# Kernel tuning notes

Measured on AMD Instinct MI355X. Metric: run time of the kernel, lower is better.

Reference implementation:

```python
import jax, jax.numpy as jnp
import numpy as np

B, P, DE, DD, DA = 256, 196, 2048, 512, 512

def setup_inputs() -> dict:
    key = jax.random.key(0)
    ks = jax.random.split(key, 8)
    s_enc = 1.0 / np.sqrt(DE)
    s_dec = 1.0 / np.sqrt(DD)
    s_att = 1.0 / np.sqrt(DA)
    return {
        "encoder_out": jax.random.normal(ks[0], (B, P, DE), dtype=jnp.float32),
        "decoder_hidden": jax.random.normal(ks[1], (B, DD), dtype=jnp.float32),
        "W_enc": jax.random.uniform(ks[2], (DE, DA), jnp.float32, -s_enc, s_enc),
        "b_enc": jax.random.uniform(ks[3], (DA,), jnp.float32, -s_enc, s_enc),
        "W_dec": jax.random.uniform(ks[4], (DD, DA), jnp.float32, -s_dec, s_dec),
        "b_dec": jax.random.uniform(ks[5], (DA,), jnp.float32, -s_dec, s_dec),
        "W_full": jax.random.uniform(ks[6], (DA, 1), jnp.float32, -s_att, s_att),
        "b_full": jax.random.uniform(ks[7], (1,), jnp.float32, -s_att, s_att),
    }

def reference(encoder_out, decoder_hidden, W_enc, b_enc, W_dec, b_dec, W_full, b_full):
    # att1: [B,P,DA]; att2: [B,DA]
    att1 = jnp.einsum('bpe,ea->bpa', encoder_out, W_enc) + b_enc
    att2 = decoder_hidden @ W_dec + b_dec
    # broadcast add + relu + project to scalar score per position
    att = jnp.einsum('bpa,a->bp', jax.nn.relu(att1 + att2[:, None, :]), W_full[:, 0]) + b_full[0]
    alpha = jax.nn.softmax(att, axis=1)  # [B,P]
    context_vector = jnp.einsum('bpe,bp->be', encoder_out, alpha)  # [B,DE]
    return (context_vector, alpha)
```

## Files before the change

kernel.cpp:

```cpp
#include <hip/hip_runtime.h>
#include <hip/hip_bf16.h>
#include <cstddef>

#define B_   256
#define P_   196
#define DE_  2048
#define DD_  512
#define DA_  512
#define M_   (B_*P_)

#define BM   64
#define KT   32

typedef __attribute__((ext_vector_type(4))) float f32x4;
typedef __attribute__((ext_vector_type(8))) short s16x8;

__global__ void pack_wenc(const float* __restrict__ W, __hip_bfloat16* __restrict__ out) {
    __shared__ float lds[KT][128 + 1];
    const int kt = blockIdx.x;
    const int n0 = blockIdx.y * 128;
    const int t  = threadIdx.x;
#pragma unroll
    for (int i = 0; i < 16; ++i) {
        int e  = t + i * 256;
        int kl = e >> 7;
        int nl = e & 127;
        lds[kl][nl] = W[(size_t)(kt * KT + kl) * DA_ + n0 + nl];
    }
    __syncthreads();
#pragma unroll
    for (int i = 0; i < 16; ++i) {
        int e  = t + i * 256;
        int nl = e >> 5;
        int kk = e & 31;
        out[((size_t)kt * DA_ + n0 + nl) * KT + kk] = __float2bfloat16(lds[kk][nl]);
    }
}

__global__ __launch_bounds__(512) void att2_kernel(
        const float* __restrict__ dh, const float* __restrict__ W_dec,
        const float* __restrict__ b_dec, const float* __restrict__ b_enc,
        float* __restrict__ att2p) {
    __shared__ float s_dh[DD_];
    const int b = blockIdx.x;
    const int a = threadIdx.x;
    s_dh[a] = dh[(size_t)b * DD_ + a];
    __syncthreads();
    float acc = 0.f;
#pragma unroll 8
    for (int k = 0; k < DD_; ++k)
        acc += s_dh[k] * W_dec[(size_t)k * DA_ + a];
    att2p[(size_t)b * DA_ + a] = acc + b_dec[a] + b_enc[a];
}

__global__ __launch_bounds__(512, 1) void gemm_att(
        const float* __restrict__ enc, const __hip_bfloat16* __restrict__ Bp,
        const float* __restrict__ att2p, const float* __restrict__ Wfull,
        const float* __restrict__ bfull, float* __restrict__ att) {
    __shared__ __hip_bfloat16 a_lds[BM * KT];
    __shared__ __hip_bfloat16 b_lds[DA_ * KT];
    __shared__ float red[BM][8];

    const int tid  = threadIdx.x;
    const int wave = tid >> 6;
    const int lane = tid & 63;
    const int g    = lane >> 4;
    const int c    = lane & 15;
    const int block_row = blockIdx.x * BM;
    const int nbase = wave * 64;

    f32x4 acc[4][4] = {};

    for (int kt = 0; kt < DE_ / KT; ++kt) {
        __syncthreads();
        {
            const int r  = tid >> 3;
            const int kk = (tid & 7) * 4;
            const float* src = enc + (size_t)(block_row + r) * DE_ + kt * KT + kk;
            f32x4 v = *reinterpret_cast<const f32x4*>(src);
            __hip_bfloat16* d = a_lds + r * KT + kk;
            d[0] = __float2bfloat16(v.x);
            d[1] = __float2bfloat16(v.y);
            d[2] = __float2bfloat16(v.z);
            d[3] = __float2bfloat16(v.w);
        }
        {
            const s16x8* src = reinterpret_cast<const s16x8*>(Bp + (size_t)kt * DA_ * KT);
            s16x8* dst = reinterpret_cast<s16x8*>(b_lds);
#pragma unroll
            for (int i = 0; i < 4; ++i)
                dst[tid + i * 512] = src[tid + i * 512];
        }
        __syncthreads();
        s16x8 afrag[4], bfrag[4];
#pragma unroll
        for (int mt = 0; mt < 4; ++mt)
            afrag[mt] = *reinterpret_cast<const s16x8*>(a_lds + (mt * 16 + c) * KT + g * 8);
#pragma unroll
        for (int nt = 0; nt < 4; ++nt)
            bfrag[nt] = *reinterpret_cast<const s16x8*>(b_lds + (nbase + nt * 16 + c) * KT + g * 8);
#pragma unroll
        for (int mt = 0; mt < 4; ++mt)
#pragma unroll
            for (int nt = 0; nt < 4; ++nt)
                acc[mt][nt] = __builtin_amdgcn_mfma_f32_16x16x32_bf16(
                                  afrag[mt], bfrag[nt], acc[mt][nt], 0, 0, 0);
    }

#pragma unroll
    for (int mt = 0; mt < 4; ++mt) {
#pragma unroll
        for (int q = 0; q < 4; ++q) {
            const int row_local = mt * 16 + g * 4 + q;
            const int R = block_row + row_local;
            const int b = R / P_;
            float s = 0.f;
#pragma unroll
            for (int nt = 0; nt < 4; ++nt) {
                const int n = nbase + nt * 16 + c;
                float v = acc[mt][nt][q] + att2p[(size_t)b * DA_ + n];
                v = fmaxf(v, 0.f);
                s += v * Wfull[n];
            }
#pragma unroll
            for (int off = 1; off < 16; off <<= 1)
                s += __shfl_xor(s, off, 64);
            if (c == 0) red[row_local][wave] = s;
        }
    }
    __syncthreads();
    if (tid < BM) {
        float t = 0.f;
#pragma unroll
        for (int w = 0; w < 8; ++w) t += red[tid][w];
        att[block_row + tid] = t + bfull[0];
    }
}

__global__ __launch_bounds__(256) void softmax_kernel(
        const float* __restrict__ att, float* __restrict__ alpha) {
    const int b = blockIdx.x;
    const int t = threadIdx.x;
    __shared__ float sred[4];
    float v = (t < P_) ? att[(size_t)b * P_ + t] : -1e30f;
    float m = v;
#pragma unroll
    for (int off = 1; off < 64; off <<= 1) m = fmaxf(m, __shfl_xor(m, off, 64));
    if ((t & 63) == 0) sred[t >> 6] = m;
    __syncthreads();
    const float mall = fmaxf(fmaxf(sred[0], sred[1]), fmaxf(sred[2], sred[3]));
    __syncthreads();
    float e = (t < P_) ? expf(v - mall) : 0.f;
    float s = e;
#pragma unroll
    for (int off = 1; off < 64; off <<= 1) s += __shfl_xor(s, off, 64);
    if ((t & 63) == 0) sred[t >> 6] = s;
    __syncthreads();
    const float stot = sred[0] + sred[1] + sred[2] + sred[3];
    if (t < P_) alpha[(size_t)b * P_ + t] = e / stot;
}

__global__ __launch_bounds__(256) void context_kernel(
        const float* __restrict__ enc, const float* __restrict__ alpha,
        float* __restrict__ ctx) {
    const int b = blockIdx.x;
    const int e = blockIdx.y * 1024 + threadIdx.x * 4;
    __shared__ float s_alpha[P_];
    if (threadIdx.x < P_) s_alpha[threadIdx.x] = alpha[(size_t)b * P_ + threadIdx.x];
    __syncthreads();
    f32x4 acc = {0.f, 0.f, 0.f, 0.f};
    const float* base = enc + (size_t)b * P_ * DE_ + e;
#pragma unroll 4
    for (int p = 0; p < P_; ++p) {
        f32x4 v = *reinterpret_cast<const f32x4*>(base + (size_t)p * DE_);
        acc += s_alpha[p] * v;
    }
    *reinterpret_cast<f32x4*>(ctx + (size_t)b * DE_ + e) = acc;
}

extern "C" void kernel_launch(void* const* d_in, const int* in_sizes, int n_in,
                              void* d_out, int out_size, void* d_ws, size_t ws_size,
                              hipStream_t stream) {
    const float* enc    = (const float*)d_in[0];
    const float* dh     = (const float*)d_in[1];
    const float* W_enc  = (const float*)d_in[2];
    const float* b_enc  = (const float*)d_in[3];
    const float* W_dec  = (const float*)d_in[4];
    const float* b_dec  = (const float*)d_in[5];
    const float* W_full = (const float*)d_in[6];
    const float* b_full = (const float*)d_in[7];

    float* out       = (float*)d_out;
    float* ctx_out   = out;
    float* alpha_out = out + (size_t)B_ * DE_;

    char* ws = (char*)d_ws;
    __hip_bfloat16* Bp = (__hip_bfloat16*)ws;
    float* att2p = (float*)(ws + 2u * 1024 * 1024);
    float* att   = (float*)(ws + 2u * 1024 * 1024 + 512u * 1024);

    pack_wenc   <<<dim3(64, 4),   256, 0, stream>>>(W_enc, Bp);
    att2_kernel <<<B_,            512, 0, stream>>>(dh, W_dec, b_dec, b_enc, att2p);
    gemm_att    <<<M_ / BM,       512, 0, stream>>>(enc, Bp, att2p, W_full, b_full, att);
    softmax_kernel<<<B_,          256, 0, stream>>>(att, alpha_out);
    context_kernel<<<dim3(B_, 2), 256, 0, stream>>>(enc, alpha_out, ctx_out);
}
```

Before: 321.2 us.

## Enlarge GEMM row tile, swizzle LDS layout, and load B via global_load_lds

The M tile grows from 64 to 112 rows, so each block does 7x4 MFMA tiles and the shared W_enc tile is reused across more rows with fewer blocks. The packed W_enc and the A tile in LDS use an XOR swizzle on the 8-element slots to cut bank conflicts. B tiles are copied straight from global memory into LDS with global_load_lds, skipping the register round trip. The epilogue preloads W_full and the att2 rows for the at most two batches a tile spans, and launch bounds now allow two blocks per CU. The risks are higher register pressure from 28 accumulator tiles and unused threads during the A load.

Measured after the change: 312.1 us. 1.03x faster.

```diff
diff --git a/kernel.cpp b/kernel.cpp
--- a/kernel.cpp
+++ b/kernel.cpp
@@ -9,11 +9,20 @@
 #define DA_  512
 #define M_   (B_*P_)
 
-#define BM   64
+#define BM   112
 #define KT   32
 
 typedef __attribute__((ext_vector_type(4))) float f32x4;
 typedef __attribute__((ext_vector_type(8))) short s16x8;
+
+static __device__ __forceinline__ short f2bf(float x) {
+    __hip_bfloat16 h = __float2bfloat16(x);
+    return *reinterpret_cast<short*>(&h);
+}
+
+#define GLOAD_LDS16(g, l) __builtin_amdgcn_global_load_lds( \
+    (const __attribute__((address_space(1))) void*)(g),     \
+    (__attribute__((address_space(3))) void*)(l), 16, 0, 0)
 
 __global__ void pack_wenc(const float* __restrict__ W, __hip_bfloat16* __restrict__ out) {
     __shared__ float lds[KT][128 + 1];
@@ -28,12 +37,19 @@
         lds[kl][nl] = W[(size_t)(kt * KT + kl) * DA_ + n0 + nl];
     }
     __syncthreads();
-#pragma unroll
-    for (int i = 0; i < 16; ++i) {
-        int e  = t + i * 256;
-        int nl = e >> 5;
-        int kk = e & 31;
-        out[((size_t)kt * DA_ + n0 + nl) * KT + kk] = __float2bfloat16(lds[kk][nl]);
+    short* o16 = reinterpret_cast<short*>(out);
+#pragma unroll
+    for (int i = 0; i < 2; ++i) {
+        int task = t + i * 256;
+        int nl   = task >> 2;
+        int s    = task & 3;
+        int n    = n0 + nl;
+        int sp   = s ^ ((n >> 1) & 3);
+        s16x8 w;
+#pragma unroll
+        for (int j = 0; j < 8; ++j)
+            w[j] = f2bf(lds[s * 8 + j][nl]);
+        *reinterpret_cast<s16x8*>(o16 + (size_t)kt * (DA_ * KT) + n * KT + sp * 8) = w;
     }
 }
 
@@ -53,7 +69,7 @@
     att2p[(size_t)b * DA_ + a] = acc + b_dec[a] + b_enc[a];
 }
 
-__global__ __launch_bounds__(512, 1) void gemm_att(
+__global__ __launch_bounds__(512, 2) void gemm_att(
         const float* __restrict__ enc, const __hip_bfloat16* __restrict__ Bp,
         const float* __restrict__ att2p, const float* __restrict__ Wfull,
         const float* __restrict__ bfull, float* __restrict__ att) {
@@ -69,58 +85,74 @@
     const int block_row = blockIdx.x * BM;
     const int nbase = wave * 64;
 
-    f32x4 acc[4][4] = {};
+    const int slot8 = (g ^ ((c >> 1) & 3)) * 8;
+
+    const int ar = tid >> 2;
+    const int aq = tid & 3;
+    const bool a_active = (tid < BM * 4);
+    __hip_bfloat16* a_dst = a_lds + ar * KT + (aq ^ ((ar >> 1) & 3)) * 8;
+    const float* a_src = enc + (size_t)(block_row + ar) * DE_ + aq * 8;
+
+    f32x4 acc[7][4] = {};
 
     for (int kt = 0; kt < DE_ / KT; ++kt) {
         __syncthreads();
         {
-            const int r  = tid >> 3;
-            const int kk = (tid & 7) * 4;
-            const float* src = enc + (size_t)(block_row + r) * DE_ + kt * KT + kk;
-            f32x4 v = *reinterpret_cast<const f32x4*>(src);
-            __hip_bfloat16* d = a_lds + r * KT + kk;
-            d[0] = __float2bfloat16(v.x);
-            d[1] = __float2bfloat16(v.y);
-            d[2] = __float2bfloat16(v.z);
-            d[3] = __float2bfloat16(v.w);
+            const char* bsrc = (const char*)Bp + (size_t)kt * (DA_ * KT * 2) + (size_t)tid * 16;
+            char*       bdst = (char*)b_lds + wave * 1024;
+#pragma unroll
+            for (int i = 0; i < 4; ++i)
+                GLOAD_LDS16(bsrc + i * 8192, bdst + i * 8192);
         }
-        {
-            const s16x8* src = reinterpret_cast<const s16x8*>(Bp + (size_t)kt * DA_ * KT);
-            s16x8* dst = reinterpret_cast<s16x8*>(b_lds);
-#pragma unroll
-            for (int i = 0; i < 4; ++i)
-                dst[tid + i * 512] = src[tid + i * 512];
+        if (a_active) {
+            f32x4 v0 = *reinterpret_cast<const f32x4*>(a_src + kt * KT);
+            f32x4 v1 = *reinterpret_cast<const f32x4*>(a_src + kt * KT + 4);
+            s16x8 w;
+            w[0] = f2bf(v0.x); w[1] = f2bf(v0.y); w[2] = f2bf(v0.z); w[3] = f2bf(v0.w);
+            w[4] = f2bf(v1.x); w[5] = f2bf(v1.y); w[6] = f2bf(v1.z); w[7] = f2bf(v1.w);
+            *reinterpret_cast<s16x8*>(a_dst) = w;
         }
         __syncthreads();
-        s16x8 afrag[4], bfrag[4];
-#pragma unroll
-        for (int mt = 0; mt < 4; ++mt)
-            afrag[mt] = *reinterpret_cast<const s16x8*>(a_lds + (mt * 16 + c) * KT + g * 8);
+        s16x8 afrag[7], bfrag[4];
+#pragma unroll
+        for (int mt = 0; mt < 7; ++mt)
+            afrag[mt] = *reinterpret_cast<const s16x8*>(a_lds + (mt * 16 + c) * KT + slot8);
 #pragma unroll
         for (int nt = 0; nt < 4; ++nt)
-            bfrag[nt] = *reinterpret_cast<const s16x8*>(b_lds + (nbase + nt * 16 + c) * KT + g * 8);
-#pragma unroll
-        for (int mt = 0; mt < 4; ++mt)
+            bfrag[nt] = *reinterpret_cast<const s16x8*>(b_lds + (nbase + nt * 16 + c) * KT + slot8);
+#pragma unroll
+        for (int mt = 0; mt < 7; ++mt)
 #pragma unroll
             for (int nt = 0; nt < 4; ++nt)
                 acc[mt][nt] = __builtin_amdgcn_mfma_f32_16x16x32_bf16(
                                   afrag[mt], bfrag[nt], acc[mt][nt], 0, 0, 0);
     }
 
-#pragma unroll
-    for (int mt = 0; mt < 4; ++mt) {
+    const int b0    = block_row / P_;
+    const int b1    = min(b0 + 1, B_ - 1);
+    const int split = (b0 + 1) * P_;
+    float wf[4], a20[4], a21[4];
+#pragma unroll
+    for (int nt = 0; nt < 4; ++nt) {
+        const int n = nbase + nt * 16 + c;
+        wf[nt]  = Wfull[n];
+        a20[nt] = att2p[(size_t)b0 * DA_ + n];
+        a21[nt] = att2p[(size_t)b1 * DA_ + n];
+    }
+#pragma unroll
+    for (int mt = 0; mt < 7; ++mt) {
 #pragma unroll
         for (int q = 0; q < 4; ++q) {
             const int row_local = mt * 16 + g * 4 + q;
             const int R = block_row + row_local;
-            const int b = R / P_;
+            const bool hi = (R >= split);
             float s = 0.f;
 #pragma unroll
             for (int nt = 0; nt < 4; ++nt) {
-                const int n = nbase + nt * 16 + c;
-                float v = acc[mt][nt][q] + att2p[(size_t)b * DA_ + n];
+                float a2 = hi ? a21[nt] : a20[nt];
+                float v  = acc[mt][nt][q] + a2;
                 v = fmaxf(v, 0.f);
-                s += v * Wfull[n];
+                s += v * wf[nt];
             }
 #pragma unroll
             for (int off = 1; off < 16; off <<= 1)
@@ -199,9 +231,9 @@
     float* att2p = (float*)(ws + 2u * 1024 * 1024);
     float* att   = (float*)(ws + 2u * 1024 * 1024 + 512u * 1024);
 
-    pack_wenc   <<<dim3(64, 4),   256, 0, stream>>>(W_enc, Bp);
-    att2_kernel <<<B_,            512, 0, stream>>>(dh, W_dec, b_dec, b_enc, att2p);
-    gemm_att    <<<M_ / BM,       512, 0, stream>>>(enc, Bp, att2p, W_full, b_full, att);
-    softmax_kernel<<<B_,          256, 0, stream>>>(att, alpha_out);
-    context_kernel<<<dim3(B_, 2), 256, 0, stream>>>(enc, alpha_out, ctx_out);
-}
+    pack_wenc   <<<dim3(64, 4),     256, 0, stream>>>(W_enc, Bp);
+    att2_kernel <<<B_,              512, 0, stream>>>(dh, W_dec, b_dec, b_enc, att2p);
+    gemm_att    <<<M_ / BM,         512, 0, stream>>>(enc, Bp, att2p, W_full, b_full, att);
+    softmax_kernel<<<B_,            256, 0, stream>>>(att, alpha_out);
+    context_kernel<<<dim3(B_, 2),   256, 0, stream>>>(enc, alpha_out, ctx_out);
+}
```
